# Optimization experiments

Hardware: AMD Instinct MI355X
Metric: run time of the kernel (lower is better)

The kernel has to match this reference:

```python
import jax, jax.numpy as jnp
import numpy as np

H = 2048            # hidden_size
IN = 64             # input_size
EMB = 8             # EMBEDDING_DIMS
LIN = IN - 4 + 4 * EMB  # 92, LSTM input width
NH = 13             # number of prediction heads
MAXO = 9            # max head output width (gear)
HEAD_OUTS = [5, 1, 1, 1, 1, 1, 1, 1, 9, 1, 3, 1, 1]
LN_EPS = 1e-5


def setup_inputs() -> dict:
    key = jax.random.key(0)
    ks = jax.random.split(key, 22)
    s = 1.0 / np.sqrt(H)
    d = {}
    d["lap_cont"] = jax.random.normal(ks[0], (1, 1, IN - 4), jnp.float32)
    d["idx"] = jax.random.randint(ks[1], (1, 1, 4), 0, 5)  # compound, driver, track, team
    d["h_s"] = 0.1 * jax.random.normal(ks[2], (2, 1, H), jnp.float32)
    d["c_s"] = 0.1 * jax.random.normal(ks[3], (2, 1, H), jnp.float32)
    d["emb_team"] = 0.02 * jax.random.normal(ks[4], (10, EMB), jnp.float32)
    d["emb_track"] = 0.02 * jax.random.normal(ks[5], (48, EMB), jnp.float32)
    d["emb_driver"] = 0.02 * jax.random.normal(ks[6], (46, EMB), jnp.float32)
    d["emb_compound"] = 0.02 * jax.random.normal(ks[7], (5, EMB), jnp.float32)
    d["W_ih0"] = s * jax.random.normal(ks[8], (4 * H, LIN), jnp.float32)
    d["W_hh0"] = s * jax.random.normal(ks[9], (4 * H, H), jnp.float32)
    d["b_ih0"] = s * jax.random.normal(ks[10], (4 * H,), jnp.float32)
    d["b_hh0"] = s * jax.random.normal(ks[11], (4 * H,), jnp.float32)
    d["W_ih1"] = s * jax.random.normal(ks[12], (4 * H, H), jnp.float32)
    d["W_hh1"] = s * jax.random.normal(ks[13], (4 * H, H), jnp.float32)
    d["b_ih1"] = s * jax.random.normal(ks[14], (4 * H,), jnp.float32)
    d["b_hh1"] = s * jax.random.normal(ks[15], (4 * H,), jnp.float32)
    d["ln_g"] = jnp.ones((H,), jnp.float32)
    d["ln_b"] = jnp.zeros((H,), jnp.float32)
    d["head_W1"] = 0.02 * jax.random.normal(ks[16], (NH, 64, H), jnp.float32)
    d["head_b1"] = 0.02 * jax.random.normal(ks[17], (NH, 64), jnp.float32)
    d["head_W2"] = 0.02 * jax.random.normal(ks[18], (NH, MAXO, 64), jnp.float32)  # padded to MAXO
    d["head_b2"] = 0.02 * jax.random.normal(ks[19], (NH, MAXO), jnp.float32)
    return d


def _lstm_cell(x, h, c, Wih, Whh, bih, bhh):
    # x:[1,in], h,c:[1,H]; PyTorch gate order i,f,g,o
    g = x @ Wih.T + bih + h @ Whh.T + bhh
    i, f, gg, o = jnp.split(g, 4, axis=-1)
    c_new = jax.nn.sigmoid(f) * c + jax.nn.sigmoid(i) * jnp.tanh(gg)
    h_new = jax.nn.sigmoid(o) * jnp.tanh(c_new)
    return h_new, c_new


def reference(lap_cont, idx, h_s, c_s, emb_team, emb_track, emb_driver, emb_compound,
              W_ih0, W_hh0, b_ih0, b_hh0, W_ih1, W_hh1, b_ih1, b_hh1,
              ln_g, ln_b, head_W1, head_b1, head_W2, head_b2):
    # Embeddings (idx order: compound, driver, track_status, team)
    comp_e = emb_compound[idx[:, :, 0]]
    drv_e = emb_driver[idx[:, :, 1]]
    trk_e = emb_track[idx[:, :, 2]]
    team_e = emb_team[idx[:, :, 3]]
    x = jnp.concatenate([lap_cont, team_e, trk_e, drv_e, comp_e], axis=-1)  # [1,1,LIN]

    x2 = x[0]  # seq_len=1 -> single cell step; [1,LIN]
    h0, c0 = _lstm_cell(x2, h_s[0], c_s[0], W_ih0, W_hh0, b_ih0, b_hh0)
    h1, c1 = _lstm_cell(h0, h_s[1], c_s[1], W_ih1, W_hh1, b_ih1, b_hh1)
    new_h = jnp.stack([h0, h1], axis=0)
    new_c = jnp.stack([c0, c1], axis=0)

    h_t = h1[None]  # [1,1,H]
    mu = jnp.mean(h_t, axis=-1, keepdims=True)
    var = jnp.mean(jnp.square(h_t - mu), axis=-1, keepdims=True)
    h_t = (h_t - mu) * jax.lax.rsqrt(var + LN_EPS) * ln_g + ln_b

    # All 13 heads fused: Dropout is identity at inference
    hid = jax.nn.relu(jnp.einsum('bsh,koh->bsko', h_t, head_W1) + head_b1)  # [1,1,13,64]
    outs = jnp.einsum('bsko,kpo->bskp', hid, head_W2) + head_b2              # [1,1,13,9]

    heads = [outs[:, :, k, :HEAD_OUTS[k]] for k in range(NH)]
    return (new_h, new_c, *heads)
```

## Files before the change

kernel.cpp:

```cpp
#include <hip/hip_runtime.h>

#define H 2048

__device__ __align__(16) float g_p1[4 * H];
__device__ __align__(16) float g_h0[H];
__device__ __align__(16) float g_h1[H];
__device__ __align__(16) float g_hid[13 * 64];

__device__ __forceinline__ float sg(float x) { return 1.f / (1.f + __expf(-x)); }

__device__ __forceinline__ float wred(float x) {
    #pragma unroll
    for (int o = 32; o > 0; o >>= 1) x += __shfl_down(x, o);
    return x;
}

__device__ __forceinline__ float dotrow(const float* __restrict__ row,
                                        const float* __restrict__ vecLDS, int lane) {
    float4 a[8];
    #pragma unroll
    for (int i = 0; i < 8; i++)
        a[i] = *reinterpret_cast<const float4*>(row + i * 256 + lane * 4);
    float acc = 0.f;
    #pragma unroll
    for (int i = 0; i < 8; i++) {
        float4 v = *reinterpret_cast<const float4*>(vecLDS + i * 256 + lane * 4);
        acc = fmaf(a[i].x, v.x, acc); acc = fmaf(a[i].y, v.y, acc);
        acc = fmaf(a[i].z, v.z, acc); acc = fmaf(a[i].w, v.w, acc);
    }
    return acc;
}

__global__ __launch_bounds__(256) void k1(
    const float* __restrict__ lap, const int* __restrict__ idx,
    const float* __restrict__ h_s, const float* __restrict__ c_s,
    const float* __restrict__ e_team, const float* __restrict__ e_trk,
    const float* __restrict__ e_drv, const float* __restrict__ e_cmp,
    const float* __restrict__ Wih0, const float* __restrict__ Whh0,
    const float* __restrict__ bih0, const float* __restrict__ bhh0,
    const float* __restrict__ Whh1, const float* __restrict__ bih1,
    const float* __restrict__ bhh1, float* __restrict__ out)
{
    __shared__ float vec[H];
    __shared__ float xsh[96];
    __shared__ float gsh[4];
    int tid = threadIdx.x, w = tid >> 6, lane = tid & 63;
    int b = blockIdx.x;
    bool l0 = b < 2048;
    const float* src = l0 ? h_s : (h_s + H);
    #pragma unroll
    for (int i = 0; i < 8; i++) vec[tid + i * 256] = src[tid + i * 256];
    if (l0 && tid < 92) {
        float v;
        if (tid < 60)      v = lap[tid];
        else if (tid < 68) v = e_team[idx[3] * 8 + tid - 60];
        else if (tid < 76) v = e_trk [idx[2] * 8 + tid - 68];
        else if (tid < 84) v = e_drv [idx[1] * 8 + tid - 76];
        else               v = e_cmp [idx[0] * 8 + tid - 84];
        xsh[tid] = v;
    }
    __syncthreads();

    if (l0) {
        int j = b;
        long row = j + (long)w * H;
        float acc = dotrow(Whh0 + row * H, vec, lane);
        const float* wr = Wih0 + row * 92;
        float p = xsh[lane] * wr[lane];
        if (lane < 28) p += xsh[lane + 64] * wr[lane + 64];
        acc = wred(acc + p);
        if (lane == 0) gsh[w] = acc + bih0[row] + bhh0[row];
        __syncthreads();
        if (tid == 0) {
            float gi = gsh[0], gf = gsh[1], gg = gsh[2], go = gsh[3];
            float cp = c_s[j];
            float cn = sg(gf) * cp + sg(gi) * tanhf(gg);
            float hn = sg(go) * tanhf(cn);
            out[j]         = hn;
            out[2 * H + j] = cn;
            g_h0[j] = hn;
        }
    } else {
        int r = (b - 2048) * 4 + w;
        float acc = dotrow(Whh1 + (long)r * H, vec, lane);
        acc = wred(acc);
        if (lane == 0) g_p1[r] = acc + bih1[r] + bhh1[r];
    }
}

__global__ __launch_bounds__(256) void k2(
    const float* __restrict__ Wih1, const float* __restrict__ c_s,
    float* __restrict__ out)
{
    __shared__ float vec[H];
    __shared__ float gsh[4];
    int tid = threadIdx.x, w = tid >> 6, lane = tid & 63;
    #pragma unroll
    for (int i = 0; i < 8; i++) vec[tid + i * 256] = g_h0[tid + i * 256];
    __syncthreads();
    int j = blockIdx.x;
    long row = j + (long)w * H;
    float acc = dotrow(Wih1 + row * H, vec, lane);
    acc = wred(acc);
    if (lane == 0) gsh[w] = acc + g_p1[row];
    __syncthreads();
    if (tid == 0) {
        float gi = gsh[0], gf = gsh[1], gg = gsh[2], go = gsh[3];
        float cp = c_s[H + j];
        float cn = sg(gf) * cp + sg(gi) * tanhf(gg);
        float hn = sg(go) * tanhf(cn);
        out[H + j]     = hn;
        out[3 * H + j] = cn;
        g_h1[j] = hn;
    }
}

__global__ __launch_bounds__(256) void k3(
    const float* __restrict__ ln_g, const float* __restrict__ ln_b,
    const float* __restrict__ W1, const float* __restrict__ b1)
{
    __shared__ float ht[H];
    __shared__ float red[8];
    __shared__ float mvs[2];
    int tid = threadIdx.x, w = tid >> 6, lane = tid & 63;
    float v[8];
    float s = 0.f, s2 = 0.f;
    #pragma unroll
    for (int i = 0; i < 8; i++) {
        float x = g_h1[tid + i * 256];
        v[i] = x; s += x; s2 += x * x;
    }
    s = wred(s); s2 = wred(s2);
    if (lane == 0) { red[w] = s; red[4 + w] = s2; }
    __syncthreads();
    if (tid == 0) {
        float ts = red[0] + red[1] + red[2] + red[3];
        float t2 = red[4] + red[5] + red[6] + red[7];
        float mu = ts / (float)H;
        float var = t2 / (float)H - mu * mu;
        mvs[0] = mu; mvs[1] = rsqrtf(var + 1e-5f);
    }
    __syncthreads();
    float mu = mvs[0], rs = mvs[1];
    #pragma unroll
    for (int i = 0; i < 8; i++) {
        int e = tid + i * 256;
        ht[e] = (v[i] - mu) * rs * ln_g[e] + ln_b[e];
    }
    __syncthreads();
    int k = blockIdx.x >> 4;
    int o = (blockIdx.x & 15) * 4 + w;
    float acc = dotrow(W1 + ((long)k * 64 + o) * H, ht, lane);
    acc = wred(acc);
    if (lane == 0) {
        float r = acc + b1[k * 64 + o];
        g_hid[k * 64 + o] = r > 0.f ? r : 0.f;
    }
}

__global__ __launch_bounds__(128) void k4(
    const float* __restrict__ W2, const float* __restrict__ b2,
    float* __restrict__ out)
{
    const int HO[13]  = {5,1,1,1,1,1,1,1,9,1,3,1,1};
    const int OFF[13] = {0,5,6,7,8,9,10,11,12,21,22,25,26};
    int t = threadIdx.x;
    if (t >= 117) return;
    int k = t / 9, p = t % 9;
    if (p >= HO[k]) return;
    const float* wr = W2 + ((long)k * 9 + p) * 64;
    const float* hp = g_hid + k * 64;
    float acc = b2[k * 9 + p];
    #pragma unroll
    for (int o = 0; o < 64; o++) acc = fmaf(hp[o], wr[o], acc);
    out[4 * H + OFF[k] + p] = acc;
}

extern "C" void kernel_launch(void* const* d_in, const int* in_sizes, int n_in,
                              void* d_out, int out_size, void* d_ws, size_t ws_size,
                              hipStream_t stream) {
    const float* lap    = (const float*)d_in[0];
    const int*   idx    = (const int*)  d_in[1];
    const float* h_s    = (const float*)d_in[2];
    const float* c_s    = (const float*)d_in[3];
    const float* e_team = (const float*)d_in[4];
    const float* e_trk  = (const float*)d_in[5];
    const float* e_drv  = (const float*)d_in[6];
    const float* e_cmp  = (const float*)d_in[7];
    const float* Wih0   = (const float*)d_in[8];
    const float* Whh0   = (const float*)d_in[9];
    const float* bih0   = (const float*)d_in[10];
    const float* bhh0   = (const float*)d_in[11];
    const float* Wih1   = (const float*)d_in[12];
    const float* Whh1   = (const float*)d_in[13];
    const float* bih1   = (const float*)d_in[14];
    const float* bhh1   = (const float*)d_in[15];
    const float* ln_g   = (const float*)d_in[16];
    const float* ln_b   = (const float*)d_in[17];
    const float* hW1    = (const float*)d_in[18];
    const float* hb1    = (const float*)d_in[19];
    const float* hW2    = (const float*)d_in[20];
    const float* hb2    = (const float*)d_in[21];
    float* out = (float*)d_out;

    k1<<<4096, 256, 0, stream>>>(lap, idx, h_s, c_s, e_team, e_trk, e_drv, e_cmp,
                                 Wih0, Whh0, bih0, bhh0, Whh1, bih1, bhh1, out);
    k2<<<2048, 256, 0, stream>>>(Wih1, c_s, out);
    k3<<<208, 256, 0, stream>>>(ln_g, ln_b, hW1, hb1);
    k4<<<1, 128, 0, stream>>>(hW2, hb2, out);
}
```

Measured before the change: 250.1 us.

## Fuse LSTM layers and heads into one cooperative persistent kernel

Replaces the four separate launches with one cooperative kernel that uses grid-wide syncs between the layer-0/Whh1 stage, the Wih1 stage, the LayerNorm+W1 head stage and the W2 stage. Each wavefront now computes all four gates for one hidden unit, loading four weight rows at once. This removes the block-level gate reduction and keeps more loads in flight. The change aims to cut launch overhead and inter-kernel gaps, at the cost of grid.sync latency and a persistent grid sized by an occupancy query, which may underfill the GPU with large register use.

```diff
diff --git a/kernel.cpp b/kernel.cpp
--- a/kernel.cpp
+++ b/kernel.cpp
@@ -1,4 +1,7 @@
 #include <hip/hip_runtime.h>
+#include <hip/hip_cooperative_groups.h>
+
+namespace cg = cooperative_groups;
 
 #define H 2048
 
@@ -7,6 +10,9 @@
 __device__ __align__(16) float g_h1[H];
 __device__ __align__(16) float g_hid[13 * 64];
 
+__device__ const int c_HO[13]  = {5,1,1,1,1,1,1,1,9,1,3,1,1};
+__device__ const int c_OFF[13] = {0,5,6,7,8,9,10,11,12,21,22,25,26};
+
 __device__ __forceinline__ float sg(float x) { return 1.f / (1.f + __expf(-x)); }
 
 __device__ __forceinline__ float wred(float x) {
@@ -15,197 +21,225 @@
     return x;
 }
 
-__device__ __forceinline__ float dotrow(const float* __restrict__ row,
-                                        const float* __restrict__ vecLDS, int lane) {
-    float4 a[8];
+__device__ __forceinline__ void dot4(const float* __restrict__ W, int j,
+                                     const float* __restrict__ vecLDS, int lane,
+                                     float acc[4]) {
+    float4 wv[4][8];
     #pragma unroll
-    for (int i = 0; i < 8; i++)
-        a[i] = *reinterpret_cast<const float4*>(row + i * 256 + lane * 4);
-    float acc = 0.f;
+    for (int q = 0; q < 4; q++) {
+        const float4* wr = reinterpret_cast<const float4*>(W + (long)(q * H + j) * H);
+        #pragma unroll
+        for (int i = 0; i < 8; i++) wv[q][i] = wr[i * 64 + lane];
+    }
     #pragma unroll
     for (int i = 0; i < 8; i++) {
-        float4 v = *reinterpret_cast<const float4*>(vecLDS + i * 256 + lane * 4);
-        acc = fmaf(a[i].x, v.x, acc); acc = fmaf(a[i].y, v.y, acc);
-        acc = fmaf(a[i].z, v.z, acc); acc = fmaf(a[i].w, v.w, acc);
-    }
-    return acc;
-}
-
-__global__ __launch_bounds__(256) void k1(
+        float4 hv = reinterpret_cast<const float4*>(vecLDS)[i * 64 + lane];
+        #pragma unroll
+        for (int q = 0; q < 4; q++) {
+            acc[q] = fmaf(wv[q][i].x, hv.x, acc[q]);
+            acc[q] = fmaf(wv[q][i].y, hv.y, acc[q]);
+            acc[q] = fmaf(wv[q][i].z, hv.z, acc[q]);
+            acc[q] = fmaf(wv[q][i].w, hv.w, acc[q]);
+        }
+    }
+}
+
+__global__ __launch_bounds__(256) void fused(
     const float* __restrict__ lap, const int* __restrict__ idx,
     const float* __restrict__ h_s, const float* __restrict__ c_s,
     const float* __restrict__ e_team, const float* __restrict__ e_trk,
     const float* __restrict__ e_drv, const float* __restrict__ e_cmp,
     const float* __restrict__ Wih0, const float* __restrict__ Whh0,
     const float* __restrict__ bih0, const float* __restrict__ bhh0,
-    const float* __restrict__ Whh1, const float* __restrict__ bih1,
-    const float* __restrict__ bhh1, float* __restrict__ out)
-{
-    __shared__ float vec[H];
-    __shared__ float xsh[96];
-    __shared__ float gsh[4];
-    int tid = threadIdx.x, w = tid >> 6, lane = tid & 63;
-    int b = blockIdx.x;
-    bool l0 = b < 2048;
-    const float* src = l0 ? h_s : (h_s + H);
-    #pragma unroll
-    for (int i = 0; i < 8; i++) vec[tid + i * 256] = src[tid + i * 256];
-    if (l0 && tid < 92) {
-        float v;
-        if (tid < 60)      v = lap[tid];
-        else if (tid < 68) v = e_team[idx[3] * 8 + tid - 60];
-        else if (tid < 76) v = e_trk [idx[2] * 8 + tid - 68];
-        else if (tid < 84) v = e_drv [idx[1] * 8 + tid - 76];
-        else               v = e_cmp [idx[0] * 8 + tid - 84];
-        xsh[tid] = v;
-    }
-    __syncthreads();
-
-    if (l0) {
-        int j = b;
-        long row = j + (long)w * H;
-        float acc = dotrow(Whh0 + row * H, vec, lane);
-        const float* wr = Wih0 + row * 92;
-        float p = xsh[lane] * wr[lane];
-        if (lane < 28) p += xsh[lane + 64] * wr[lane + 64];
-        acc = wred(acc + p);
-        if (lane == 0) gsh[w] = acc + bih0[row] + bhh0[row];
-        __syncthreads();
-        if (tid == 0) {
-            float gi = gsh[0], gf = gsh[1], gg = gsh[2], go = gsh[3];
-            float cp = c_s[j];
-            float cn = sg(gf) * cp + sg(gi) * tanhf(gg);
-            float hn = sg(go) * tanhf(cn);
-            out[j]         = hn;
-            out[2 * H + j] = cn;
-            g_h0[j] = hn;
-        }
-    } else {
-        int r = (b - 2048) * 4 + w;
-        float acc = dotrow(Whh1 + (long)r * H, vec, lane);
-        acc = wred(acc);
-        if (lane == 0) g_p1[r] = acc + bih1[r] + bhh1[r];
-    }
-}
-
-__global__ __launch_bounds__(256) void k2(
-    const float* __restrict__ Wih1, const float* __restrict__ c_s,
-    float* __restrict__ out)
-{
-    __shared__ float vec[H];
-    __shared__ float gsh[4];
-    int tid = threadIdx.x, w = tid >> 6, lane = tid & 63;
-    #pragma unroll
-    for (int i = 0; i < 8; i++) vec[tid + i * 256] = g_h0[tid + i * 256];
-    __syncthreads();
-    int j = blockIdx.x;
-    long row = j + (long)w * H;
-    float acc = dotrow(Wih1 + row * H, vec, lane);
-    acc = wred(acc);
-    if (lane == 0) gsh[w] = acc + g_p1[row];
-    __syncthreads();
-    if (tid == 0) {
-        float gi = gsh[0], gf = gsh[1], gg = gsh[2], go = gsh[3];
-        float cp = c_s[H + j];
-        float cn = sg(gf) * cp + sg(gi) * tanhf(gg);
-        float hn = sg(go) * tanhf(cn);
-        out[H + j]     = hn;
-        out[3 * H + j] = cn;
-        g_h1[j] = hn;
-    }
-}
-
-__global__ __launch_bounds__(256) void k3(
+    const float* __restrict__ Wih1, const float* __restrict__ Whh1,
+    const float* __restrict__ bih1, const float* __restrict__ bhh1,
     const float* __restrict__ ln_g, const float* __restrict__ ln_b,
-    const float* __restrict__ W1, const float* __restrict__ b1)
-{
-    __shared__ float ht[H];
-    __shared__ float red[8];
-    __shared__ float mvs[2];
-    int tid = threadIdx.x, w = tid >> 6, lane = tid & 63;
-    float v[8];
-    float s = 0.f, s2 = 0.f;
-    #pragma unroll
-    for (int i = 0; i < 8; i++) {
-        float x = g_h1[tid + i * 256];
-        v[i] = x; s += x; s2 += x * x;
-    }
-    s = wred(s); s2 = wred(s2);
-    if (lane == 0) { red[w] = s; red[4 + w] = s2; }
-    __syncthreads();
-    if (tid == 0) {
-        float ts = red[0] + red[1] + red[2] + red[3];
-        float t2 = red[4] + red[5] + red[6] + red[7];
-        float mu = ts / (float)H;
-        float var = t2 / (float)H - mu * mu;
-        mvs[0] = mu; mvs[1] = rsqrtf(var + 1e-5f);
-    }
-    __syncthreads();
-    float mu = mvs[0], rs = mvs[1];
-    #pragma unroll
-    for (int i = 0; i < 8; i++) {
-        int e = tid + i * 256;
-        ht[e] = (v[i] - mu) * rs * ln_g[e] + ln_b[e];
-    }
-    __syncthreads();
-    int k = blockIdx.x >> 4;
-    int o = (blockIdx.x & 15) * 4 + w;
-    float acc = dotrow(W1 + ((long)k * 64 + o) * H, ht, lane);
-    acc = wred(acc);
-    if (lane == 0) {
-        float r = acc + b1[k * 64 + o];
-        g_hid[k * 64 + o] = r > 0.f ? r : 0.f;
-    }
-}
-
-__global__ __launch_bounds__(128) void k4(
+    const float* __restrict__ W1, const float* __restrict__ b1,
     const float* __restrict__ W2, const float* __restrict__ b2,
     float* __restrict__ out)
 {
-    const int HO[13]  = {5,1,1,1,1,1,1,1,9,1,3,1,1};
-    const int OFF[13] = {0,5,6,7,8,9,10,11,12,21,22,25,26};
-    int t = threadIdx.x;
-    if (t >= 117) return;
-    int k = t / 9, p = t % 9;
-    if (p >= HO[k]) return;
-    const float* wr = W2 + ((long)k * 9 + p) * 64;
-    const float* hp = g_hid + k * 64;
-    float acc = b2[k * 9 + p];
-    #pragma unroll
-    for (int o = 0; o < 64; o++) acc = fmaf(hp[o], wr[o], acc);
-    out[4 * H + OFF[k] + p] = acc;
+    __shared__ float vec[2 * H];
+    __shared__ float xsh[96];
+    __shared__ float red[8];
+    __shared__ float mvs[2];
+    cg::grid_group grid = cg::this_grid();
+
+    int tid = threadIdx.x, w = tid >> 6, lane = tid & 63;
+    int nw = gridDim.x * 4;
+    int gw = blockIdx.x * 4 + w;
+
+    {
+        float4* v4 = reinterpret_cast<float4*>(vec);
+        const float4* s4 = reinterpret_cast<const float4*>(h_s);
+        #pragma unroll
+        for (int i = 0; i < 4; i++) v4[tid + i * 256] = s4[tid + i * 256];
+        if (tid < 92) {
+            float v;
+            if (tid < 60)      v = lap[tid];
+            else if (tid < 68) v = e_team[idx[3] * 8 + tid - 60];
+            else if (tid < 76) v = e_trk [idx[2] * 8 + tid - 68];
+            else if (tid < 84) v = e_drv [idx[1] * 8 + tid - 76];
+            else               v = e_cmp [idx[0] * 8 + tid - 84];
+            xsh[tid] = v;
+        }
+    }
+    __syncthreads();
+
+    for (int u = gw; u < 4096; u += nw) {
+        float acc[4] = {0.f, 0.f, 0.f, 0.f};
+        if (u < 2048) {
+            int j = u;
+            dot4(Whh0, j, vec, lane, acc);
+            #pragma unroll
+            for (int q = 0; q < 4; q++) {
+                const float* wr = Wih0 + (long)(q * H + j) * 92;
+                float p = xsh[lane] * wr[lane];
+                if (lane < 28) p = fmaf(xsh[lane + 64], wr[lane + 64], p);
+                acc[q] += p;
+            }
+            float bs[4];
+            #pragma unroll
+            for (int q = 0; q < 4; q++) bs[q] = bih0[q * H + j] + bhh0[q * H + j];
+            #pragma unroll
+            for (int q = 0; q < 4; q++) acc[q] = wred(acc[q]);
+            if (lane == 0) {
+                float gi = acc[0] + bs[0], gf = acc[1] + bs[1];
+                float gg = acc[2] + bs[2], go = acc[3] + bs[3];
+                float cp = c_s[j];
+                float cn = sg(gf) * cp + sg(gi) * tanhf(gg);
+                float hn = sg(go) * tanhf(cn);
+                out[j]         = hn;
+                out[2 * H + j] = cn;
+                g_h0[j] = hn;
+            }
+        } else {
+            int j = u - 2048;
+            dot4(Whh1, j, vec + H, lane, acc);
+            float bs[4];
+            #pragma unroll
+            for (int q = 0; q < 4; q++) bs[q] = bih1[q * H + j] + bhh1[q * H + j];
+            #pragma unroll
+            for (int q = 0; q < 4; q++) acc[q] = wred(acc[q]);
+            if (lane == 0) {
+                #pragma unroll
+                for (int q = 0; q < 4; q++) g_p1[q * H + j] = acc[q] + bs[q];
+            }
+        }
+    }
+    __threadfence();
+    grid.sync();
+
+    {
+        float4* v4 = reinterpret_cast<float4*>(vec);
+        const float4* s4 = reinterpret_cast<const float4*>(g_h0);
+        #pragma unroll
+        for (int i = 0; i < 2; i++) v4[tid + i * 256] = s4[tid + i * 256];
+    }
+    __syncthreads();
+    for (int c = gw; c < 2048; c += nw) {
+        float acc[4] = {0.f, 0.f, 0.f, 0.f};
+        dot4(Wih1, c, vec, lane, acc);
+        float ps[4];
+        #pragma unroll
+        for (int q = 0; q < 4; q++) ps[q] = g_p1[q * H + c];
+        #pragma unroll
+        for (int q = 0; q < 4; q++) acc[q] = wred(acc[q]);
+        if (lane == 0) {
+            float gi = acc[0] + ps[0], gf = acc[1] + ps[1];
+            float gg = acc[2] + ps[2], go = acc[3] + ps[3];
+            float cp = c_s[H + c];
+            float cn = sg(gf) * cp + sg(gi) * tanhf(gg);
+            float hn = sg(go) * tanhf(cn);
+            out[H + c]     = hn;
+            out[3 * H + c] = cn;
+            g_h1[c] = hn;
+        }
+    }
+    __threadfence();
+    grid.sync();
+
+    bool cwork = ((blockIdx.x * 4) < 832) || (nw < 832);
+    if (cwork) {
+        const float4* s4 = reinterpret_cast<const float4*>(g_h1);
+        float4* v4 = reinterpret_cast<float4*>(vec);
+        float4 h0v = s4[tid], h1v = s4[tid + 256];
+        float s  = h0v.x + h0v.y + h0v.z + h0v.w + h1v.x + h1v.y + h1v.z + h1v.w;
+        float s2 = h0v.x*h0v.x + h0v.y*h0v.y + h0v.z*h0v.z + h0v.w*h0v.w
+                 + h1v.x*h1v.x + h1v.y*h1v.y + h1v.z*h1v.z + h1v.w*h1v.w;
+        s = wred(s); s2 = wred(s2);
+        if (lane == 0) { red[w] = s; red[4 + w] = s2; }
+        __syncthreads();
+        if (tid == 0) {
+            float ts = red[0] + red[1] + red[2] + red[3];
+            float t2 = red[4] + red[5] + red[6] + red[7];
+            float mu = ts / (float)H;
+            float var = t2 / (float)H - mu * mu;
+            mvs[0] = mu; mvs[1] = rsqrtf(var + 1e-5f);
+        }
+        __syncthreads();
+        float mu = mvs[0], rs = mvs[1];
+        const float4* g4 = reinterpret_cast<const float4*>(ln_g);
+        const float4* b4 = reinterpret_cast<const float4*>(ln_b);
+        float4 ga = g4[tid], gb = g4[tid + 256];
+        float4 ba = b4[tid], bb = b4[tid + 256];
+        float4 o0, o1;
+        o0.x = (h0v.x - mu) * rs * ga.x + ba.x;  o0.y = (h0v.y - mu) * rs * ga.y + ba.y;
+        o0.z = (h0v.z - mu) * rs * ga.z + ba.z;  o0.w = (h0v.w - mu) * rs * ga.w + ba.w;
+        o1.x = (h1v.x - mu) * rs * gb.x + bb.x;  o1.y = (h1v.y - mu) * rs * gb.y + bb.y;
+        o1.z = (h1v.z - mu) * rs * gb.z + bb.z;  o1.w = (h1v.w - mu) * rs * gb.w + bb.w;
+        v4[tid] = o0; v4[tid + 256] = o1;
+        __syncthreads();
+        for (int r = gw; r < 832; r += nw) {
+            const float4* wr = reinterpret_cast<const float4*>(W1 + (long)r * H);
+            float4 wv[8];
+            #pragma unroll
+            for (int i = 0; i < 8; i++) wv[i] = wr[i * 64 + lane];
+            float a = 0.f;
+            #pragma unroll
+            for (int i = 0; i < 8; i++) {
+                float4 hh = reinterpret_cast<const float4*>(vec)[i * 64 + lane];
+                a = fmaf(wv[i].x, hh.x, a); a = fmaf(wv[i].y, hh.y, a);
+                a = fmaf(wv[i].z, hh.z, a); a = fmaf(wv[i].w, hh.w, a);
+            }
+            a = wred(a);
+            if (lane == 0) {
+                float t = a + b1[r];
+                g_hid[r] = t > 0.f ? t : 0.f;
+            }
+        }
+    }
+    __threadfence();
+    grid.sync();
+
+    for (int r = gw; r < 117; r += nw) {
+        int k = r / 9, p = r - k * 9;
+        if (p < c_HO[k]) {
+            float wv = W2[((long)(k * 9 + p)) * 64 + lane];
+            float hh = g_hid[k * 64 + lane];
+            float a = wred(wv * hh);
+            if (lane == 0) out[4 * H + c_OFF[k] + p] = a + b2[k * 9 + p];
+        }
+    }
 }
 
 extern "C" void kernel_launch(void* const* d_in, const int* in_sizes, int n_in,
                               void* d_out, int out_size, void* d_ws, size_t ws_size,
                               hipStream_t stream) {
-    const float* lap    = (const float*)d_in[0];
-    const int*   idx    = (const int*)  d_in[1];
-    const float* h_s    = (const float*)d_in[2];
-    const float* c_s    = (const float*)d_in[3];
-    const float* e_team = (const float*)d_in[4];
-    const float* e_trk  = (const float*)d_in[5];
-    const float* e_drv  = (const float*)d_in[6];
-    const float* e_cmp  = (const float*)d_in[7];
-    const float* Wih0   = (const float*)d_in[8];
-    const float* Whh0   = (const float*)d_in[9];
-    const float* bih0   = (const float*)d_in[10];
-    const float* bhh0   = (const float*)d_in[11];
-    const float* Wih1   = (const float*)d_in[12];
-    const float* Whh1   = (const float*)d_in[13];
-    const float* bih1   = (const float*)d_in[14];
-    const float* bhh1   = (const float*)d_in[15];
-    const float* ln_g   = (const float*)d_in[16];
-    const float* ln_b   = (const float*)d_in[17];
-    const float* hW1    = (const float*)d_in[18];
-    const float* hb1    = (const float*)d_in[19];
-    const float* hW2    = (const float*)d_in[20];
-    const float* hb2    = (const float*)d_in[21];
-    float* out = (float*)d_out;
-
-    k1<<<4096, 256, 0, stream>>>(lap, idx, h_s, c_s, e_team, e_trk, e_drv, e_cmp,
-                                 Wih0, Whh0, bih0, bhh0, Whh1, bih1, bhh1, out);
-    k2<<<2048, 256, 0, stream>>>(Wih1, c_s, out);
-    k3<<<208, 256, 0, stream>>>(ln_g, ln_b, hW1, hb1);
-    k4<<<1, 128, 0, stream>>>(hW2, hb2, out);
-}
+    static int grid = 0;
+    if (grid == 0) {
+        int nb = 0;
+        if (hipOccupancyMaxActiveBlocksPerMultiprocessor(&nb, fused, 256, 0) != hipSuccess || nb <= 0)
+            nb = 2;
+        long cap = (long)nb * 256;
+        grid = cap < 1024 ? (int)cap : 1024;
+    }
+
+    void* in22[22];
+    for (int i = 0; i < 22; i++) in22[i] = d_in[i];
+    void* outp = d_out;
+    void* args[23];
+    for (int i = 0; i < 22; i++) args[i] = &in22[i];
+    args[22] = &outp;
+
+    hipLaunchCooperativeKernel(fused, dim3(grid), dim3(256), args, 0, stream);
+}
```

New measurement: 450.7 us. 1.8x slower.
